# Kernel optimization log

Hardware: AMD Instinct MI355X
Metric: run time of the kernel (lower is better)

## Reference

```python
import jax, jax.numpy as jnp
import numpy as np

D_IN = 1024
D_OUT = 1024
NUM_HEADS = 16
HEAD_DIM = D_OUT // NUM_HEADS


def setup_inputs() -> dict:
    key = jax.random.key(0)
    ks = jax.random.split(key, 9)
    s = 0.02
    return {
        "x": jax.random.normal(ks[0], (2, 2048, D_IN), dtype=jnp.float32),
        "Wq": jax.random.normal(ks[1], (D_IN, D_OUT), dtype=jnp.float32) * s,
        "bq": jnp.zeros((D_OUT,), dtype=jnp.float32),
        "Wk": jax.random.normal(ks[2], (D_IN, D_OUT), dtype=jnp.float32) * s,
        "bk": jnp.zeros((D_OUT,), dtype=jnp.float32),
        "Wv": jax.random.normal(ks[3], (D_IN, D_OUT), dtype=jnp.float32) * s,
        "bv": jnp.zeros((D_OUT,), dtype=jnp.float32),
        "Wo": jax.random.normal(ks[4], (D_OUT, D_OUT), dtype=jnp.float32) * s,
        "bo": jnp.zeros((D_OUT,), dtype=jnp.float32),
    }


def reference(x, Wq, bq, Wk, bk, Wv, bv, Wo, bo):
    B, S, _ = x.shape
    H, Dh = NUM_HEADS, HEAD_DIM
    q = (x @ Wq + bq).reshape(B, S, H, Dh).transpose(0, 2, 1, 3)  # bhsd
    k = (x @ Wk + bk).reshape(B, S, H, Dh).transpose(0, 2, 1, 3)
    v = (x @ Wv + bv).reshape(B, S, H, Dh).transpose(0, 2, 1, 3)
    scores = jnp.einsum("bhqd,bhkd->bhqk", q, k) * (Dh ** -0.5)
    causal = jnp.tril(jnp.ones((S, S), dtype=bool))
    scores = jnp.where(causal, scores, jnp.float32(-jnp.inf))
    w = jax.nn.softmax(scores, axis=-1)
    ctx = jnp.einsum("bhqk,bhkd->bhqd", w, v)
    ctx = ctx.transpose(0, 2, 1, 3).reshape(B, S, H * Dh)
    return ctx @ Wo + bo
```

## Files before the change

### kernel.cpp

```cpp
#include <hip/hip_runtime.h>
#include <cmath>

#define D_IN 1024
#define D_OUT 1024
#define NUM_HEADS 16
#define HEAD_DIM 64
#define BATCH 2
#define SEQ 2048
#define GK 1024
#define KT 32
#define NT_K (GK / 64)

typedef __attribute__((ext_vector_type(8))) short short8;
typedef __attribute__((ext_vector_type(4))) short short4v;
typedef __attribute__((ext_vector_type(4))) float float4v;
typedef __attribute__((ext_vector_type(16))) float f32x16;
typedef __attribute__((ext_vector_type(2))) int int2v;

__device__ __forceinline__ unsigned short f2bf(float f) {
  unsigned int u = __builtin_bit_cast(unsigned int, f);
  unsigned int r = (u + 0x7FFFu + ((u >> 16) & 1u)) >> 16;
  return (unsigned short)r;
}
__device__ __forceinline__ float bf2f(unsigned short h) {
  return __builtin_bit_cast(float, (unsigned int)h << 16);
}

__device__ __forceinline__ unsigned int cvtpk(float lo, float hi) {
  unsigned int r;
  asm("v_cvt_pk_bf16_f32 %0, %1, %2" : "=v"(r) : "v"(lo), "v"(hi));
  return r;
}

__device__ __forceinline__ void async_copy16(void* lds, const void* g) {
  __builtin_amdgcn_global_load_lds(
      (const __attribute__((address_space(1))) unsigned int*)g,
      (__attribute__((address_space(3))) unsigned int*)lds, 16, 0, 0);
}

__global__ __launch_bounds__(256) void prep(
    const float* __restrict__ x, const float* __restrict__ Wq,
    const float* __restrict__ Wk, const float* __restrict__ Wv,
    const float* __restrict__ Wo, unsigned short* __restrict__ xb,
    unsigned short* __restrict__ wqkv_t, unsigned short* __restrict__ wo_t) {
  const int z = blockIdx.z;
  if (z == 4) {
    const int bid = blockIdx.y * 32 + blockIdx.x;
    const size_t i0 = ((size_t)bid * 256 + threadIdx.x) * 16;
#pragma unroll
    for (int half = 0; half < 2; ++half) {
      const size_t o = i0 + half * 8;
      float4 a = *(const float4*)(x + o);
      float4 b = *(const float4*)(x + o + 4);
      union { unsigned int d[4]; short8 v; } t;
      t.d[0] = cvtpk(a.x, a.y); t.d[1] = cvtpk(a.z, a.w);
      t.d[2] = cvtpk(b.x, b.y); t.d[3] = cvtpk(b.z, b.w);
      *(short8*)(xb + o) = t.v;
    }
    return;
  }
  const float* W = (z == 0) ? Wq : (z == 1) ? Wk : (z == 2) ? Wv : Wo;
  unsigned short* out = (z < 3) ? (wqkv_t + (size_t)z * 1024 * 1024) : wo_t;

  __shared__ float T[32][33];
  const int r = threadIdx.x >> 3;
  const int c4 = (threadIdx.x & 7) << 2;
  const int k0 = blockIdx.x * 32, n0 = blockIdx.y * 32;

  float4 v = *(const float4*)(W + (size_t)(k0 + r) * 1024 + n0 + c4);
  T[r][c4 + 0] = v.x; T[r][c4 + 1] = v.y; T[r][c4 + 2] = v.z; T[r][c4 + 3] = v.w;
  __syncthreads();

  union { unsigned short u[4]; short4v v4; } o;
#pragma unroll
  for (int i = 0; i < 4; ++i) o.u[i] = f2bf(T[c4 + i][r]);
  *(short4v*)(out + (size_t)(n0 + r) * 1024 + k0 + c4) = o.v4;
}

__device__ __forceinline__ void stage_tile(
    const unsigned short* __restrict__ A, const unsigned short* __restrict__ Bt,
    unsigned short* S, int buf, int bm, int bn, int k0, int wave, int lane) {
  unsigned short* As = S + buf * 16384;
  unsigned short* Bs = As + 8192;
#pragma unroll
  for (int t = 0; t < 4; ++t) {
    const int c = (wave * 4 + t) * 64 + lane;
    const int srow = c >> 3;
    const int sgc = ((c & 7) ^ (srow & 7)) * 8;
    async_copy16(As + (size_t)c * 8, A + (size_t)(bm + srow) * GK + k0 + sgc);
  }
#pragma unroll
  for (int t = 0; t < 4; ++t) {
    const int c = (wave * 4 + t) * 64 + lane;
    const int srow = c >> 3;
    const int sgc = ((c & 7) ^ (srow & 7)) * 8;
    async_copy16(Bs + (size_t)c * 8, Bt + (size_t)(bn + srow) * GK + k0 + sgc);
  }
}

__device__ __forceinline__ void gemm_core(
    const unsigned short* __restrict__ A, const unsigned short* __restrict__ Bt,
    unsigned short* S, int bm, int bn, float4v acc[4][4]) {
  const int tid = threadIdx.x;
  const int wave = tid >> 6, lane = tid & 63;
  const int quad = lane >> 4, l16 = lane & 15;
  const int wr = wave >> 1, wc = wave & 1;
  const int sw = l16 & 7;

  stage_tile(A, Bt, S, 0, bm, bn, 0, wave, lane);

  for (int t = 0; t < NT_K; ++t) {
    if (t + 1 < NT_K) {
      stage_tile(A, Bt, S, (t + 1) & 1, bm, bn, (t + 1) * 64, wave, lane);
      asm volatile("s_waitcnt vmcnt(8)" ::: "memory");
    } else {
      asm volatile("s_waitcnt vmcnt(0)" ::: "memory");
    }
    __builtin_amdgcn_sched_barrier(0);
    __builtin_amdgcn_s_barrier();
    __builtin_amdgcn_sched_barrier(0);

    const unsigned short* Asc = S + (t & 1) * 16384;
    const unsigned short* Bsc = Asc + 8192;
#pragma unroll
    for (int h = 0; h < 2; ++h) {
      short8 af[4], bfr[4];
#pragma unroll
      for (int i = 0; i < 4; ++i) {
        const int row = wr * 64 + i * 16 + l16;
        af[i] = *(const short8*)&Asc[((size_t)row * 8 + ((h * 4 + quad) ^ sw)) * 8];
      }
#pragma unroll
      for (int j = 0; j < 4; ++j) {
        const int row = wc * 64 + j * 16 + l16;
        bfr[j] = *(const short8*)&Bsc[((size_t)row * 8 + ((h * 4 + quad) ^ sw)) * 8];
      }
#pragma unroll
      for (int i = 0; i < 4; ++i)
#pragma unroll
        for (int j = 0; j < 4; ++j)
          acc[i][j] = __builtin_amdgcn_mfma_f32_16x16x32_bf16(af[i], bfr[j], acc[i][j], 0, 0, 0);
    }

    __builtin_amdgcn_sched_barrier(0);
    __builtin_amdgcn_s_barrier();
    __builtin_amdgcn_sched_barrier(0);
  }
}

__global__ __launch_bounds__(256) void gemm_qkv(
    const unsigned short* __restrict__ A, const unsigned short* __restrict__ Bt,
    const float* __restrict__ bq, const float* __restrict__ bk,
    const float* __restrict__ bv,
    unsigned short* __restrict__ qbuf, unsigned short* __restrict__ kblk,
    unsigned short* __restrict__ vblk) {
  __shared__ unsigned short SMEM[2 * 128 * 64 * 2];
  const int tid = threadIdx.x;
  const int wave = tid >> 6, lane = tid & 63;
  const int quad = lane >> 4, l16 = lane & 15;
  const int wr = wave >> 1, wc = wave & 1;

  const int lid = blockIdx.y * 32 + blockIdx.x;
  const int nid = (lid & 7) * 96 + (lid >> 3);
  const int bm = (nid & 31) * 128, bn = (nid >> 5) * 128;

  float4v acc[4][4] = {};
  gemm_core(A, Bt, SMEM, bm, bn, acc);

  __syncthreads();

  const int seg = bn >> 10;
  const int nb0 = bn & 1023;
  const float* bias = (seg == 0) ? bq : (seg == 1) ? bk : bv;
  const float scale = (seg == 0) ? 0.18033688011112043f : 1.0f;

#pragma unroll
  for (int j = 0; j < 4; ++j) {
    const int nl = wc * 64 + j * 16 + l16;
    const float bsv = bias[nb0 + nl];
#pragma unroll
    for (int i = 0; i < 4; ++i) {
#pragma unroll
      for (int r = 0; r < 4; ++r) {
        const int ml = wr * 64 + i * 16 + quad * 4 + r;
        SMEM[ml * 136 + nl] = f2bf((acc[i][j][r] + bsv) * scale);
      }
    }
  }
  __syncthreads();

  const int b = bm >> 11;
  const int s0 = bm & 2047;

  if (seg == 0) {
#pragma unroll
    for (int it = 0; it < 8; ++it) {
      const int linear = it * 256 + tid;
      const int d3 = linear & 7;
      const int sl = (linear >> 3) & 127;
      const int h = linear >> 10;
      const short8 vv = *(const short8*)&SMEM[sl * 136 + h * 64 + d3 * 8];
      const int bh = b * NUM_HEADS + (nb0 >> 6) + h;
      *(short8*)&qbuf[((size_t)bh * SEQ + s0 + sl) * HEAD_DIM + d3 * 8] = vv;
    }
  } else if (seg == 1) {
#pragma unroll
    for (int it = 0; it < 8; ++it) {
      const int linear = it * 256 + tid;
      const int key = linear & 31;
      const int hb = (linear >> 5) & 1;
      const int f = (linear >> 6) & 3;
      const int st = (linear >> 8) & 3;
      const int h = linear >> 10;
      const int ml = st * 32 + key;
      const int nl = h * 64 + f * 16 + hb * 8;
      const short8 vv = *(const short8*)&SMEM[ml * 136 + nl];
      const int bh = b * NUM_HEADS + (nb0 >> 6) + h;
      const int stg = (s0 >> 5) + st;
      *(short8*)&kblk[((size_t)bh * 64 + stg) * 2048 + f * 512 + hb * 256 + key * 8] = vv;
    }
  } else {
#pragma unroll
    for (int it = 0; it < 8; ++it) {
      const int linear = it * 256 + tid;
      const int d31 = linear & 31;
      const int s8 = (linear >> 5) & 1;
      const int dt = (linear >> 6) & 1;
      const int kk = (linear >> 7) & 1;
      const int st = (linear >> 8) & 3;
      const int h = linear >> 10;
      const int nl = h * 64 + dt * 32 + d31;
      const int mlb = st * 32 + kk * 16 + s8 * 8;
      union { unsigned short u[8]; short8 v; } vv;
#pragma unroll
      for (int s0i = 0; s0i < 8; ++s0i)
        vv.u[s0i] = SMEM[(mlb + s0i) * 136 + nl];
      const int bh = b * NUM_HEADS + (nb0 >> 6) + h;
      const int stg = (s0 >> 5) + st;
      *(short8*)&vblk[((size_t)bh * 64 + stg) * 2048 + (kk * 2 + dt) * 512 +
                      s8 * 256 + d31 * 8] = vv.v;
    }
  }
}

__global__ __launch_bounds__(256) void gemm_out(
    const unsigned short* __restrict__ A, const unsigned short* __restrict__ Bt,
    const float* __restrict__ bo, float* __restrict__ out) {
  __shared__ unsigned short S[2 * 128 * 64 * 2];
  const int wave = threadIdx.x >> 6, lane = threadIdx.x & 63;
  const int quad = lane >> 4, l16 = lane & 15;
  const int wr = wave >> 1, wc = wave & 1;

  const int lid = blockIdx.y * 32 + blockIdx.x;
  const int nid = (lid & 7) * 32 + (lid >> 3);
  const int bm = (nid & 31) * 128, bn = (nid >> 5) * 128;

  float4v acc[4][4] = {};
  gemm_core(A, Bt, S, bm, bn, acc);

#pragma unroll
  for (int j = 0; j < 4; ++j) {
    const int n = bn + wc * 64 + j * 16 + l16;
    const float bsv = bo[n];
#pragma unroll
    for (int i = 0; i < 4; ++i) {
#pragma unroll
      for (int r = 0; r < 4; ++r) {
        const int m = bm + wr * 64 + i * 16 + quad * 4 + r;
        out[(size_t)m * D_OUT + n] = acc[i][j][r] + bsv;
      }
    }
  }
}

#define OBS 72

__global__ __launch_bounds__(256) void attn_kernel(
    const unsigned short* __restrict__ qf, const unsigned short* __restrict__ kblk,
    const unsigned short* __restrict__ vblk, unsigned short* __restrict__ ctx) {
  __shared__ unsigned short OB[4 * 64 * OBS];
  __shared__ float LL[4 * 64];

  const int id = blockIdx.x;
  const int bh = id & 31;
  const int j = 31 - (id >> 5);
  const int qw0 = j * 64;
  const int tid = threadIdx.x;
  const int w = tid >> 6;
  const int lane = tid & 63;
  const int l32 = lane & 31;
  const int hi = lane >> 5;

  const int nt = 2 * j + 2;
  const int qch = (nt + 3) >> 2;
  const int t0 = w * qch;
  const int t1 = min(nt, t0 + qch);

  const size_t bh_base = (size_t)bh * SEQ * HEAD_DIM;
  const unsigned short* kb = kblk + bh_base + (size_t)lane * 8;
  const unsigned short* vb = vblk + bh_base + (size_t)lane * 8;

  short8 qfr[2][4];
#pragma unroll
  for (int qt = 0; qt < 2; ++qt) {
    const unsigned short* qrow =
        qf + bh_base + (size_t)(qw0 + qt * 32 + l32) * HEAD_DIM + hi * 8;
#pragma unroll
    for (int f = 0; f < 4; ++f) qfr[qt][f] = *(const short8*)(qrow + f * 16);
  }

  f32x16 O[2][2] = {};
  float l_part[2] = {};

  if (t0 < t1) {
    short8 kA[4], vA[4], kB[4], vB[4];

    auto load = [&](int kt, short8 kd[4], short8 vd[4]) {
      const size_t base = (size_t)kt * 2048;
#pragma unroll
      for (int f = 0; f < 4; ++f) kd[f] = *(const short8*)(kb + base + f * 512);
#pragma unroll
      for (int f = 0; f < 4; ++f) vd[f] = *(const short8*)(vb + base + f * 512);
    };

    auto step = [&](int kt, const short8 kd[4], const short8 vd[4]) {
#pragma unroll
      for (int qt = 0; qt < 2; ++qt) {
        if (qt == 0 && kt > 2 * j) continue;
        const bool masked = (kt == 2 * j + qt);
        f32x16 s = {};
#pragma unroll
        for (int f = 0; f < 4; ++f)
          s = __builtin_amdgcn_mfma_f32_32x32x16_bf16(kd[f], qfr[qt][f], s, 0, 0, 0);

        float p[16];
#pragma unroll
        for (int g = 0; g < 4; ++g)
#pragma unroll
          for (int r = 0; r < 4; ++r) {
            float sv = s[g * 4 + r];
            if (masked) {
              const int krow = r + 8 * g + 4 * hi;
              sv = (krow <= l32) ? sv : -1e30f;
            }
            const float pv = __builtin_exp2f(sv);
            p[g * 4 + r] = pv;
            l_part[qt] += pv;
          }

        unsigned int c[8];
#pragma unroll
        for (int g = 0; g < 4; ++g) {
          c[g * 2 + 0] = cvtpk(p[g * 4 + 0], p[g * 4 + 1]);
          c[g * 2 + 1] = cvtpk(p[g * 4 + 2], p[g * 4 + 3]);
        }
        {
          int2v r0 = __builtin_amdgcn_permlane32_swap((int)c[0], (int)c[2], false, false);
          c[0] = (unsigned int)r0.x; c[2] = (unsigned int)r0.y;
          int2v r1 = __builtin_amdgcn_permlane32_swap((int)c[1], (int)c[3], false, false);
          c[1] = (unsigned int)r1.x; c[3] = (unsigned int)r1.y;
          int2v r2 = __builtin_amdgcn_permlane32_swap((int)c[4], (int)c[6], false, false);
          c[4] = (unsigned int)r2.x; c[6] = (unsigned int)r2.y;
          int2v r3 = __builtin_amdgcn_permlane32_swap((int)c[5], (int)c[7], false, false);
          c[5] = (unsigned int)r3.x; c[7] = (unsigned int)r3.y;
        }
        union { unsigned int d[4]; short8 v; } pa0, pa1;
        pa0.d[0] = c[0]; pa0.d[1] = c[1]; pa0.d[2] = c[2]; pa0.d[3] = c[3];
        pa1.d[0] = c[4]; pa1.d[1] = c[5]; pa1.d[2] = c[6]; pa1.d[3] = c[7];

        O[qt][0] = __builtin_amdgcn_mfma_f32_32x32x16_bf16(pa0.v, vd[0], O[qt][0], 0, 0, 0);
        O[qt][1] = __builtin_amdgcn_mfma_f32_32x32x16_bf16(pa0.v, vd[1], O[qt][1], 0, 0, 0);
        O[qt][0] = __builtin_amdgcn_mfma_f32_32x32x16_bf16(pa1.v, vd[2], O[qt][0], 0, 0, 0);
        O[qt][1] = __builtin_amdgcn_mfma_f32_32x32x16_bf16(pa1.v, vd[3], O[qt][1], 0, 0, 0);
      }
    };

    load(t0, kA, vA);
    int kt = t0;
    while (true) {
      const bool lastA = (kt == t1 - 1);
      if (!lastA) load(kt + 1, kB, vB);
      step(kt, kA, vA);
      if (lastA) break;
      ++kt;
      const bool lastB = (kt == t1 - 1);
      if (!lastB) load(kt + 1, kA, vA);
      step(kt, kB, vB);
      if (lastB) break;
      ++kt;
    }
  }

#pragma unroll
  for (int qt = 0; qt < 2; ++qt) {
    const float lsum = l_part[qt] + __shfl_xor(l_part[qt], 32);
    if (hi == 0) LL[w * 64 + qt * 32 + l32] = lsum;
#pragma unroll
    for (int g = 0; g < 4; ++g)
#pragma unroll
      for (int r = 0; r < 4; ++r) {
        const int reg = g * 4 + r;
        const int row = qt * 32 + r + 8 * g + 4 * hi;
        OB[(w * 64 + row) * OBS + l32] = f2bf(O[qt][0][reg]);
        OB[(w * 64 + row) * OBS + 32 + l32] = f2bf(O[qt][1][reg]);
      }
  }

  __syncthreads();

  const int b = bh >> 4, h = bh & 15;
#pragma unroll
  for (int rep = 0; rep < 2; ++rep) {
    const int idx = rep * 256 + tid;
    const int row = idx >> 3;
    const int col0 = (idx & 7) * 8;
    float acc[8] = {};
#pragma unroll
    for (int u = 0; u < 4; ++u) {
      const short8 t = *(const short8*)&OB[(u * 64 + row) * OBS + col0];
#pragma unroll
      for (int i = 0; i < 8; ++i) acc[i] += bf2f((unsigned short)t[i]);
    }
    const float inv =
        1.0f / (LL[row] + LL[64 + row] + LL[128 + row] + LL[192 + row]);
    union { unsigned short u[8]; short8 v; } o;
#pragma unroll
    for (int i = 0; i < 8; ++i) o.u[i] = f2bf(acc[i] * inv);
    const int qg = qw0 + row;
    *(short8*)(ctx + ((size_t)b * SEQ + qg) * D_OUT + h * HEAD_DIM + col0) = o.v;
  }
}

extern "C" void kernel_launch(void* const* d_in, const int* in_sizes, int n_in,
                              void* d_out, int out_size, void* d_ws, size_t ws_size,
                              hipStream_t stream) {
  const float* x  = (const float*)d_in[0];
  const float* Wq = (const float*)d_in[1];
  const float* bq = (const float*)d_in[2];
  const float* Wk = (const float*)d_in[3];
  const float* bk = (const float*)d_in[4];
  const float* Wv = (const float*)d_in[5];
  const float* bv = (const float*)d_in[6];
  const float* Wo = (const float*)d_in[7];
  const float* bo = (const float*)d_in[8];
  float* out = (float*)d_out;

  const int M = BATCH * SEQ;
  unsigned short* xb     = (unsigned short*)d_ws;
  unsigned short* wqkv_t = xb + (size_t)M * D_IN;
  unsigned short* wo_t   = wqkv_t + (size_t)3 * D_OUT * D_IN;
  unsigned short* qb     = wo_t + (size_t)D_OUT * D_OUT;
  unsigned short* kblk   = qb + (size_t)M * D_OUT;
  unsigned short* vblk   = kblk + (size_t)M * D_OUT;
  unsigned short* cb     = vblk + (size_t)M * D_OUT;

  prep<<<dim3(32, 32, 5), 256, 0, stream>>>(x, Wq, Wk, Wv, Wo, xb, wqkv_t, wo_t);
  gemm_qkv<<<dim3(M / 128, 3 * D_OUT / 128), 256, 0, stream>>>(
      xb, wqkv_t, bq, bk, bv, qb, kblk, vblk);
  attn_kernel<<<dim3(32 * 32), 256, 0, stream>>>(qb, kblk, vblk, cb);
  gemm_out<<<dim3(M / 128, D_OUT / 128), 256, 0, stream>>>(cb, wo_t, bo, out);
}
```

Before: 178.3 us.

## Pair mirrored 32-row query tiles per block for balanced causal attention work

Each attention block now processes two 32-row query tiles, a and 63-a, instead of one contiguous 64-row tile. Every block therefore does roughly equal causal work, and the four waves interleave key tiles with stride 4 instead of taking contiguous chunks. This removes the load imbalance between blocks near the start and end of the sequence, and between waves. The cost is noncontiguous output rows, and the two query tiles share loaded K/V only for key tiles up to a.

```diff
diff --git a/kernel.cpp b/kernel.cpp
--- a/kernel.cpp
+++ b/kernel.cpp
@@ -283,36 +283,35 @@
 
   const int id = blockIdx.x;
   const int bh = id & 31;
-  const int j = 31 - (id >> 5);
-  const int qw0 = j * 64;
+  const int pr = id >> 5;
+  const int a = pr;
+  const int b = 63 - pr;
   const int tid = threadIdx.x;
   const int w = tid >> 6;
   const int lane = tid & 63;
   const int l32 = lane & 31;
   const int hi = lane >> 5;
 
-  const int nt = 2 * j + 2;
-  const int qch = (nt + 3) >> 2;
-  const int t0 = w * qch;
-  const int t1 = min(nt, t0 + qch);
-
   const size_t bh_base = (size_t)bh * SEQ * HEAD_DIM;
   const unsigned short* kb = kblk + bh_base + (size_t)lane * 8;
   const unsigned short* vb = vblk + bh_base + (size_t)lane * 8;
 
   short8 qfr[2][4];
-#pragma unroll
-  for (int qt = 0; qt < 2; ++qt) {
-    const unsigned short* qrow =
-        qf + bh_base + (size_t)(qw0 + qt * 32 + l32) * HEAD_DIM + hi * 8;
-#pragma unroll
-    for (int f = 0; f < 4; ++f) qfr[qt][f] = *(const short8*)(qrow + f * 16);
+  {
+    const int q0[2] = {a * 32, b * 32};
+#pragma unroll
+    for (int qt = 0; qt < 2; ++qt) {
+      const unsigned short* qrow =
+          qf + bh_base + (size_t)(q0[qt] + l32) * HEAD_DIM + hi * 8;
+#pragma unroll
+      for (int f = 0; f < 4; ++f) qfr[qt][f] = *(const short8*)(qrow + f * 16);
+    }
   }
 
   f32x16 O[2][2] = {};
   float l_part[2] = {};
 
-  if (t0 < t1) {
+  {
     short8 kA[4], vA[4], kB[4], vB[4];
 
     auto load = [&](int kt, short8 kd[4], short8 vd[4]) {
@@ -323,71 +322,71 @@
       for (int f = 0; f < 4; ++f) vd[f] = *(const short8*)(vb + base + f * 512);
     };
 
+    auto unit = [&](int qt, bool masked, const short8 kd[4], const short8 vd[4]) {
+      f32x16 s = {};
+#pragma unroll
+      for (int f = 0; f < 4; ++f)
+        s = __builtin_amdgcn_mfma_f32_32x32x16_bf16(kd[f], qfr[qt][f], s, 0, 0, 0);
+
+      float p[16];
+#pragma unroll
+      for (int g = 0; g < 4; ++g)
+#pragma unroll
+        for (int r = 0; r < 4; ++r) {
+          float sv = s[g * 4 + r];
+          if (masked) {
+            const int krow = r + 8 * g + 4 * hi;
+            sv = (krow <= l32) ? sv : -1e30f;
+          }
+          const float pv = __builtin_exp2f(sv);
+          p[g * 4 + r] = pv;
+          l_part[qt] += pv;
+        }
+
+      unsigned int c[8];
+#pragma unroll
+      for (int g = 0; g < 4; ++g) {
+        c[g * 2 + 0] = cvtpk(p[g * 4 + 0], p[g * 4 + 1]);
+        c[g * 2 + 1] = cvtpk(p[g * 4 + 2], p[g * 4 + 3]);
+      }
+      {
+        int2v r0 = __builtin_amdgcn_permlane32_swap((int)c[0], (int)c[2], false, false);
+        c[0] = (unsigned int)r0.x; c[2] = (unsigned int)r0.y;
+        int2v r1 = __builtin_amdgcn_permlane32_swap((int)c[1], (int)c[3], false, false);
+        c[1] = (unsigned int)r1.x; c[3] = (unsigned int)r1.y;
+        int2v r2 = __builtin_amdgcn_permlane32_swap((int)c[4], (int)c[6], false, false);
+        c[4] = (unsigned int)r2.x; c[6] = (unsigned int)r2.y;
+        int2v r3 = __builtin_amdgcn_permlane32_swap((int)c[5], (int)c[7], false, false);
+        c[5] = (unsigned int)r3.x; c[7] = (unsigned int)r3.y;
+      }
+      union { unsigned int d[4]; short8 v; } pa0, pa1;
+      pa0.d[0] = c[0]; pa0.d[1] = c[1]; pa0.d[2] = c[2]; pa0.d[3] = c[3];
+      pa1.d[0] = c[4]; pa1.d[1] = c[5]; pa1.d[2] = c[6]; pa1.d[3] = c[7];
+
+      O[qt][0] = __builtin_amdgcn_mfma_f32_32x32x16_bf16(pa0.v, vd[0], O[qt][0], 0, 0, 0);
+      O[qt][1] = __builtin_amdgcn_mfma_f32_32x32x16_bf16(pa0.v, vd[1], O[qt][1], 0, 0, 0);
+      O[qt][0] = __builtin_amdgcn_mfma_f32_32x32x16_bf16(pa1.v, vd[2], O[qt][0], 0, 0, 0);
+      O[qt][1] = __builtin_amdgcn_mfma_f32_32x32x16_bf16(pa1.v, vd[3], O[qt][1], 0, 0, 0);
+    };
+
     auto step = [&](int kt, const short8 kd[4], const short8 vd[4]) {
-#pragma unroll
-      for (int qt = 0; qt < 2; ++qt) {
-        if (qt == 0 && kt > 2 * j) continue;
-        const bool masked = (kt == 2 * j + qt);
-        f32x16 s = {};
-#pragma unroll
-        for (int f = 0; f < 4; ++f)
-          s = __builtin_amdgcn_mfma_f32_32x32x16_bf16(kd[f], qfr[qt][f], s, 0, 0, 0);
-
-        float p[16];
-#pragma unroll
-        for (int g = 0; g < 4; ++g)
-#pragma unroll
-          for (int r = 0; r < 4; ++r) {
-            float sv = s[g * 4 + r];
-            if (masked) {
-              const int krow = r + 8 * g + 4 * hi;
-              sv = (krow <= l32) ? sv : -1e30f;
-            }
-            const float pv = __builtin_exp2f(sv);
-            p[g * 4 + r] = pv;
-            l_part[qt] += pv;
-          }
-
-        unsigned int c[8];
-#pragma unroll
-        for (int g = 0; g < 4; ++g) {
-          c[g * 2 + 0] = cvtpk(p[g * 4 + 0], p[g * 4 + 1]);
-          c[g * 2 + 1] = cvtpk(p[g * 4 + 2], p[g * 4 + 3]);
-        }
-        {
-          int2v r0 = __builtin_amdgcn_permlane32_swap((int)c[0], (int)c[2], false, false);
-          c[0] = (unsigned int)r0.x; c[2] = (unsigned int)r0.y;
-          int2v r1 = __builtin_amdgcn_permlane32_swap((int)c[1], (int)c[3], false, false);
-          c[1] = (unsigned int)r1.x; c[3] = (unsigned int)r1.y;
-          int2v r2 = __builtin_amdgcn_permlane32_swap((int)c[4], (int)c[6], false, false);
-          c[4] = (unsigned int)r2.x; c[6] = (unsigned int)r2.y;
-          int2v r3 = __builtin_amdgcn_permlane32_swap((int)c[5], (int)c[7], false, false);
-          c[5] = (unsigned int)r3.x; c[7] = (unsigned int)r3.y;
-        }
-        union { unsigned int d[4]; short8 v; } pa0, pa1;
-        pa0.d[0] = c[0]; pa0.d[1] = c[1]; pa0.d[2] = c[2]; pa0.d[3] = c[3];
-        pa1.d[0] = c[4]; pa1.d[1] = c[5]; pa1.d[2] = c[6]; pa1.d[3] = c[7];
-
-        O[qt][0] = __builtin_amdgcn_mfma_f32_32x32x16_bf16(pa0.v, vd[0], O[qt][0], 0, 0, 0);
-        O[qt][1] = __builtin_amdgcn_mfma_f32_32x32x16_bf16(pa0.v, vd[1], O[qt][1], 0, 0, 0);
-        O[qt][0] = __builtin_amdgcn_mfma_f32_32x32x16_bf16(pa1.v, vd[2], O[qt][0], 0, 0, 0);
-        O[qt][1] = __builtin_amdgcn_mfma_f32_32x32x16_bf16(pa1.v, vd[3], O[qt][1], 0, 0, 0);
-      }
+      unit(1, kt == b, kd, vd);
+      if (kt <= a) unit(0, kt == a, kd, vd);
     };
 
-    load(t0, kA, vA);
-    int kt = t0;
+    load(w, kA, vA);
+    int kt = w;
     while (true) {
-      const bool lastA = (kt == t1 - 1);
-      if (!lastA) load(kt + 1, kB, vB);
+      const bool lastA = (kt + 4 > b);
+      if (!lastA) load(kt + 4, kB, vB);
       step(kt, kA, vA);
       if (lastA) break;
-      ++kt;
-      const bool lastB = (kt == t1 - 1);
-      if (!lastB) load(kt + 1, kA, vA);
+      kt += 4;
+      const bool lastB = (kt + 4 > b);
+      if (!lastB) load(kt + 4, kA, vA);
       step(kt, kB, vB);
       if (lastB) break;
-      ++kt;
+      kt += 4;
     }
   }
 
@@ -408,7 +407,7 @@
 
   __syncthreads();
 
-  const int b = bh >> 4, h = bh & 15;
+  const int bb = bh >> 4, h = bh & 15;
 #pragma unroll
   for (int rep = 0; rep < 2; ++rep) {
     const int idx = rep * 256 + tid;
@@ -426,8 +425,8 @@
     union { unsigned short u[8]; short8 v; } o;
 #pragma unroll
     for (int i = 0; i < 8; ++i) o.u[i] = f2bf(acc[i] * inv);
-    const int qg = qw0 + row;
-    *(short8*)(ctx + ((size_t)b * SEQ + qg) * D_OUT + h * HEAD_DIM + col0) = o.v;
+    const int qg = (row < 32) ? (a * 32 + row) : (b * 32 + row - 32);
+    *(short8*)(ctx + ((size_t)bb * SEQ + qg) * D_OUT + h * HEAD_DIM + col0) = o.v;
   }
 }
 
```

Measured after the change: 182.5 us. +2.4%, slower.
